# Optimization experiments

Measured on AMD Instinct MI355X. Metric: run time of the kernel, lower is better.

The kernel has to match this reference:

```python
import jax, jax.numpy as jnp
import numpy as np

EMBED_DIM = 1024
NUM_HEADS = 16
WINDOW = 128  # one-sided window length w; total span 2w+1


def setup_inputs() -> dict:
    key = jax.random.key(0)
    ks = jax.random.split(key, 9)
    D = EMBED_DIM
    x = jax.random.normal(ks[0], (2, 8192, D), dtype=jnp.float32)
    s = 0.02
    Wq = jax.random.normal(ks[1], (D, D), dtype=jnp.float32) * s
    bq = jax.random.normal(ks[2], (D,), dtype=jnp.float32) * s
    Wk = jax.random.normal(ks[3], (D, D), dtype=jnp.float32) * s
    bk = jax.random.normal(ks[4], (D,), dtype=jnp.float32) * s
    Wv = jax.random.normal(ks[5], (D, D), dtype=jnp.float32) * s
    bv = jax.random.normal(ks[6], (D,), dtype=jnp.float32) * s
    Wo = jax.random.normal(ks[7], (D, D), dtype=jnp.float32) * s
    bo = jax.random.normal(ks[8], (D,), dtype=jnp.float32) * s
    return {"x": x, "Wq": Wq, "bq": bq, "Wk": Wk, "bk": bk,
            "Wv": Wv, "bv": bv, "Wo": Wo, "bo": bo}


def _sliding_window_attention(x, Wq, bq, Wk, bk, Wv, bv, Wo, bo):
    B, S, D = x.shape
    H, w = NUM_HEADS, WINDOW
    hd = D // H
    bs = w            # block size = window_length; 3 blocks cover [i-w, i+w]
    nb = S // bs

    def proj(W, b):
        y = x @ W.T + b                              # torch Linear: x @ W.T + b
        return y.reshape(B, S, H, hd).transpose(0, 2, 1, 3)  # [B,H,S,hd]

    q = proj(Wq, bq)
    k = proj(Wk, bk)
    v = proj(Wv, bv)

    qb = q.reshape(B, H, nb, bs, hd)
    # pad K/V with one zero block on each side, then build 3-block contexts
    pad = ((0, 0), (0, 0), (bs, bs), (0, 0))
    kp = jnp.pad(k, pad).reshape(B, H, nb + 2, bs, hd)
    vp = jnp.pad(v, pad).reshape(B, H, nb + 2, bs, hd)
    k_ctx = jnp.concatenate([kp[:, :, :-2], kp[:, :, 1:-1], kp[:, :, 2:]], axis=3)  # [B,H,nb,3bs,hd]
    v_ctx = jnp.concatenate([vp[:, :, :-2], vp[:, :, 1:-1], vp[:, :, 2:]], axis=3)

    scale = 1.0 / np.sqrt(hd).astype(np.float32)
    scores = jnp.einsum('bhnqd,bhnkd->bhnqk', qb, k_ctx) * scale  # [B,H,nb,bs,3bs]

    # band mask: |k_pos - q_pos| <= w, and k_pos in [0, S)
    q_off = jnp.arange(bs)
    k_off = jnp.arange(3 * bs)
    rel = k_off[None, :] - bs - q_off[:, None]                # [bs,3bs]
    win_ok = jnp.abs(rel) <= w
    k_pos = (jnp.arange(nb)[:, None, None] - 1) * bs + k_off[None, None, :]
    valid = (k_pos >= 0) & (k_pos < S)                        # [nb,1,3bs]
    mask = win_ok[None] & valid                               # [nb,bs,3bs]

    scores = jnp.where(mask[None, None], scores, jnp.float32(-jnp.inf))
    weights = jax.nn.softmax(scores, axis=-1)

    out = jnp.einsum('bhnqk,bhnkd->bhnqd', weights, v_ctx)    # [B,H,nb,bs,hd]
    out = out.reshape(B, H, S, hd).transpose(0, 2, 1, 3).reshape(B, S, D)
    return out @ Wo.T + bo


def reference(x, Wq, bq, Wk, bk, Wv, bv, Wo, bo):
    return _sliding_window_attention(x, Wq, bq, Wk, bk, Wv, bv, Wo, bo)
```

## Files before the change

kernel.cpp:

```cpp
#include <hip/hip_runtime.h>

typedef __attribute__((ext_vector_type(4))) float f32x4;
typedef __attribute__((ext_vector_type(8))) short s16x8;

#define MFMA16(a, b, c) __builtin_amdgcn_mfma_f32_16x16x32_bf16((a), (b), (c), 0, 0, 0)

__device__ __forceinline__ unsigned short f2bf_bits(float f) {
  unsigned int u = __float_as_uint(f);
  unsigned int r = (u + 0x7fffu + ((u >> 16) & 1u)) >> 16;
  return (unsigned short)r;
}

__device__ __forceinline__ void gl_lds16(const void* g, void* l) {
  __builtin_amdgcn_global_load_lds((const __attribute__((address_space(1))) void*)g,
                                   (__attribute__((address_space(3))) void*)l, 16, 0, 0);
}

__global__ __launch_bounds__(256) void f2bf_kernel(const float* __restrict__ in,
                                                   unsigned short* __restrict__ out, int n4) {
  int idx = blockIdx.x * 256 + threadIdx.x;
  int stride = gridDim.x * 256;
  for (int i = idx; i < n4; i += stride) {
    float4 v = ((const float4*)in)[i];
    ushort4 o;
    o.x = f2bf_bits(v.x); o.y = f2bf_bits(v.y);
    o.z = f2bf_bits(v.z); o.w = f2bf_bits(v.w);
    ((ushort4*)out)[i] = o;
  }
}

__global__ __launch_bounds__(256) void f2bf_w4(const float* __restrict__ w0,
                                               const float* __restrict__ w1,
                                               const float* __restrict__ w2,
                                               const float* __restrict__ w3,
                                               unsigned short* __restrict__ o0,
                                               unsigned short* __restrict__ o1,
                                               unsigned short* __restrict__ o2,
                                               unsigned short* __restrict__ o3) {
  const int s = blockIdx.y;
  const float* in = (s == 0) ? w0 : (s == 1) ? w1 : (s == 2) ? w2 : w3;
  unsigned short* out = (s == 0) ? o0 : (s == 1) ? o1 : (s == 2) ? o2 : o3;
  int i = blockIdx.x * 256 + threadIdx.x;
  float4 v = ((const float4*)in)[i];
  ushort4 o;
  o.x = f2bf_bits(v.x); o.y = f2bf_bits(v.y);
  o.z = f2bf_bits(v.z); o.w = f2bf_bits(v.w);
  ((ushort4*)out)[i] = o;
}


#define S_BARRIER asm volatile("s_barrier" ::: "memory")
#define WAIT_LGKM0 asm volatile("s_waitcnt lgkmcnt(0)" ::: "memory")
#define SCHED_FENCE __builtin_amdgcn_sched_barrier(0)

#define STAGE_HALF(gsrc, ldst)                                                   \
  {                                                                              \
    _Pragma("unroll") for (int i_ = 0; i_ < 2; ++i_) {                           \
      const int ci_ = tid + 512 * i_;                                            \
      const int r_ = ci_ >> 3;                                                   \
      const int c_ = (ci_ & 7) ^ (r_ & 7);                                       \
      gl_lds16((gsrc) + (size_t)r_ * 1024 + c_ * 8, (ldst) + ci_ * 8);           \
    }                                                                            \
  }

#define LDA8(dst, mf_, ks_)                                                      \
  dst = *(const s16x8*)&Ahalf[(((mf_) * 16 + l15) * 8 +                          \
                               (((ks_) * 4 + quad) ^ (l15 & 7))) * 8]
#define LDB8(dst, nf_, ks_)                                                      \
  dst = *(const s16x8*)&Bhalf[((bro + (nf_) * 16 + l15) * 8 +                    \
                               (((ks_) * 4 + quad) ^ (l15 & 7))) * 8]

#define MF_BLOCK(MBASE, NBASE)                                                   \
  _Pragma("unroll") for (int m_ = 0; m_ < 4; ++m_)                               \
    _Pragma("unroll") for (int n_ = 0; n_ < 2; ++n_) {                           \
      acc[(MBASE) + m_][(NBASE) + n_] =                                          \
          MFMA16(af[m_][0], bf[(NBASE) + n_][0], acc[(MBASE) + m_][(NBASE) + n_]); \
      acc[(MBASE) + m_][(NBASE) + n_] =                                          \
          MFMA16(af[m_][1], bf[(NBASE) + n_][1], acc[(MBASE) + m_][(NBASE) + n_]); \
    }

#define GEMM256_CORE(Ab_, Bb_)                                                   \
  f32x4 acc[8][4];                                                               \
  _Pragma("unroll") for (int mi = 0; mi < 8; ++mi)                               \
      _Pragma("unroll") for (int ni = 0; ni < 4; ++ni)                           \
          acc[mi][ni] = (f32x4){0.f, 0.f, 0.f, 0.f};                             \
  {                                                                              \
    s16x8 af[4][2], bf[4][2];                                                    \
                 \
    STAGE_HALF((Ab_), &Al[0][0][0]);                                             \
    STAGE_HALF((Ab_) + 128 * 1024, &Al[0][1][0]);                                \
    STAGE_HALF((Bb_), &Bl[0][0][0]);                                             \
    STAGE_HALF((Bb_) + 128 * 1024, &Bl[0][1][0]);                                \
    STAGE_HALF((Bb_) + 64, &Bl[1][0][0]);                                        \
    STAGE_HALF((Bb_) + 128 * 1024 + 64, &Bl[1][1][0]);                           \
    asm volatile("s_waitcnt vmcnt(4)" ::: "memory");         \
    S_BARRIER;                                                                   \
    _Pragma("unroll 2") for (int T = 0; T < 16; ++T) {                           \
      const int buf_ = T & 1, obuf_ = buf_ ^ 1;                                  \
      const unsigned short* Ahalf = &Al[buf_][wm][0];                            \
      const unsigned short* Bhalf = &Bl[buf_][wn >> 1][0];                       \
          \
      _Pragma("unroll") for (int m_ = 0; m_ < 4; ++m_) {                         \
        LDA8(af[m_][0], m_, 0); LDA8(af[m_][1], m_, 1);                          \
      }                                                                          \
      _Pragma("unroll") for (int n_ = 0; n_ < 2; ++n_) {                         \
        LDB8(bf[n_][0], n_, 0); LDB8(bf[n_][1], n_, 1);                          \
      }                                                                          \
      if (T < 15) STAGE_HALF((Ab_) + (size_t)(T + 1) * 64, &Al[obuf_][0][0]);    \
      S_BARRIER; WAIT_LGKM0; SCHED_FENCE;                                        \
      __builtin_amdgcn_s_setprio(1);                                             \
      MF_BLOCK(0, 0)                                                             \
      __builtin_amdgcn_s_setprio(0);                                             \
      S_BARRIER;                                                                 \
                   \
      _Pragma("unroll") for (int n_ = 2; n_ < 4; ++n_) {                         \
        LDB8(bf[n_][0], n_, 0); LDB8(bf[n_][1], n_, 1);                          \
      }                                                                          \
      if (T < 15)                                                                \
        STAGE_HALF((Ab_) + 128 * 1024 + (size_t)(T + 1) * 64, &Al[obuf_][1][0]); \
      S_BARRIER; WAIT_LGKM0; SCHED_FENCE;                                        \
      __builtin_amdgcn_s_setprio(1);                                             \
      MF_BLOCK(0, 2)                                                             \
      __builtin_amdgcn_s_setprio(0);                                             \
      S_BARRIER;                                                                 \
                   \
      _Pragma("unroll") for (int m_ = 0; m_ < 4; ++m_) {                         \
        LDA8(af[m_][0], 4 + m_, 0); LDA8(af[m_][1], 4 + m_, 1);                  \
      }                                                                          \
      if (T < 14) STAGE_HALF((Bb_) + (size_t)(T + 2) * 64, &Bl[buf_][0][0]);     \
      S_BARRIER; WAIT_LGKM0; SCHED_FENCE;                                        \
      __builtin_amdgcn_s_setprio(1);                                             \
      MF_BLOCK(4, 0)                                                             \
      __builtin_amdgcn_s_setprio(0);                                             \
      S_BARRIER;                                                                 \
                  \
      if (T < 14)                                                                \
        STAGE_HALF((Bb_) + 128 * 1024 + (size_t)(T + 2) * 64, &Bl[buf_][1][0]);  \
      if (T < 14) {                                                              \
        asm volatile("s_waitcnt vmcnt(4)" ::: "memory");                         \
      } else {                                                                   \
        asm volatile("s_waitcnt vmcnt(0)" ::: "memory");                         \
      }                                                                          \
      S_BARRIER; SCHED_FENCE;                                                    \
      __builtin_amdgcn_s_setprio(1);                                             \
      MF_BLOCK(4, 2)                                                             \
      __builtin_amdgcn_s_setprio(0);                                             \
      S_BARRIER;                                                                 \
    }                                                                            \
  }

__global__ __launch_bounds__(512, 2) void gemm_qkv(const unsigned short* __restrict__ A,
                                                   const unsigned short* __restrict__ Wq,
                                                   const unsigned short* __restrict__ Wk,
                                                   const unsigned short* __restrict__ Wv,
                                                   const float* __restrict__ bq,
                                                   const float* __restrict__ bk,
                                                   const float* __restrict__ bv,
                                                   unsigned short* __restrict__ Qo,
                                                   unsigned short* __restrict__ Ko,
                                                   unsigned short* __restrict__ Vt) {
  __shared__ unsigned short Al[2][2][8192];
  __shared__ unsigned short Bl[2][2][8192];
  const int tid = threadIdx.x;
  const int lane = tid & 63, wave = tid >> 6;
  const int l15 = lane & 15, quad = lane >> 4;
  const int wm = wave >> 2, wn = wave & 3;
  const int bro = (wn & 1) * 64;
  const int bx = blockIdx.x;
  const int sel = blockIdx.y >> 2, byl = blockIdx.y & 3;

  const unsigned short* W = (sel == 0) ? Wq : (sel == 1) ? Wk : Wv;
  const float* bias = (sel == 0) ? bq : (sel == 1) ? bk : bv;
  const unsigned short* Ab = A + (size_t)bx * 256 * 1024;
  const unsigned short* Bb = W + (size_t)byl * 256 * 1024;

  GEMM256_CORE(Ab, Bb)

#pragma unroll
  for (int nf = 0; nf < 4; ++nf) {
    const int cn = byl * 256 + wn * 64 + nf * 16 + l15;
    const float bj = bias[cn];
#pragma unroll
    for (int mf = 0; mf < 8; ++mf) {
      const int r0 = bx * 256 + wm * 128 + mf * 16 + quad * 4;
#pragma unroll
      for (int r = 0; r < 4; ++r) {
        const int row = r0 + r;
        const float v = acc[mf][nf][r] + bj;
        if (sel == 0) {
          Qo[(size_t)row * 1024 + cn] = f2bf_bits(v);
        } else if (sel == 1) {
          Ko[(size_t)row * 1024 + cn] = f2bf_bits(v);
        } else {
          Vt[((size_t)(row >> 13) * 1024 + cn) * 8192 + (row & 8191)] = f2bf_bits(v);
        }
      }
    }
  }
}

__global__ __launch_bounds__(512, 2) void gemm_out(const unsigned short* __restrict__ A,
                                                   const unsigned short* __restrict__ B,
                                                   const float* __restrict__ bias,
                                                   float* __restrict__ Cf) {
  __shared__ unsigned short Al[2][2][8192];
  __shared__ unsigned short Bl[2][2][8192];
  const int tid = threadIdx.x;
  const int lane = tid & 63, wave = tid >> 6;
  const int l15 = lane & 15, quad = lane >> 4;
  const int wm = wave >> 2, wn = wave & 3;
  const int bro = (wn & 1) * 64;
  const int bx = blockIdx.x;

  const unsigned short* Ab = A + (size_t)bx * 256 * 1024;
  const unsigned short* Bb = B + (size_t)blockIdx.y * 256 * 1024;

  GEMM256_CORE(Ab, Bb)

#pragma unroll
  for (int nf = 0; nf < 4; ++nf) {
    const int cn = blockIdx.y * 256 + wn * 64 + nf * 16 + l15;
    const float bj = bias[cn];
#pragma unroll
    for (int mf = 0; mf < 8; ++mf) {
      const int r0 = bx * 256 + wm * 128 + mf * 16 + quad * 4;
#pragma unroll
      for (int r = 0; r < 4; ++r) Cf[(size_t)(r0 + r) * 1024 + cn] = acc[mf][nf][r] + bj;
    }
  }
}

__global__ __launch_bounds__(256, 3) void attn_kernel(const unsigned short* __restrict__ Q,
                                                      const unsigned short* __restrict__ Km,
                                                      const unsigned short* __restrict__ Vt,
                                                      unsigned short* __restrict__ O) {
  const int n = blockIdx.x;
  const int bh = blockIdx.y;
  const int b = bh >> 4, h = bh & 15;
  const int tid = threadIdx.x, lane = tid & 63, wave = tid >> 6;
  const int l15 = lane & 15, quad = lane >> 4;

  __shared__ unsigned short Kl[384 * 64];
  __shared__ unsigned short Ps[4][16 * 40];

  const int base_row = n * 128 - 128;

  for (int i = 0; i < 12; ++i) {
    const int c = i * 256 + tid;
    const int row = c >> 3;
    const int qc = (c & 7) ^ (row & 7);
    int gr = base_row + row;
    gr = min(max(gr, 0), 8191);
    gl_lds16(Km + (size_t)(b * 8192 + gr) * 1024 + h * 64 + qc * 8, &Kl[c * 8]);
  }
  __syncthreads();

  const unsigned short* Vbase = Vt + (size_t)bh * 64 * 8192;
  unsigned short* strip = &Ps[wave][0];

  for (int mt = 0; mt < 2; ++mt) {
    const int qt = wave * 2 + mt;
    const int q0 = n * 128 + qt * 16;
    const int qp = q0 + l15;

    const unsigned short* qptr = Q + (size_t)(b * 8192 + qp) * 1024 + h * 64 + quad * 8;
    const s16x8 bq0 = *(const s16x8*)qptr;
    const s16x8 bq1 = *(const s16x8*)(qptr + 32);

    f32x4 o[4];
#pragma unroll
    for (int dt = 0; dt < 4; ++dt) o[dt] = (f32x4){0.f, 0.f, 0.f, 0.f};
    float lsum = 0.f;

    const int krel0 = qt * 16;

#pragma unroll 1
    for (int p = 0; p < 9; ++p) {
      f32x4 st[2];
#pragma unroll
      for (int tt = 0; tt < 2; ++tt) {
        int rel = krel0 + p * 32 + tt * 16 + l15;
        int rr = min(rel, 383);
        const int ro = rr * 8;
        const int sw = rr & 7;
        const s16x8 ka0 = *(const s16x8*)&Kl[(ro + (quad ^ sw)) * 8];
        const s16x8 ka1 = *(const s16x8*)&Kl[(ro + ((4 + quad) ^ sw)) * 8];
        f32x4 a = (f32x4){0.f, 0.f, 0.f, 0.f};
        a = MFMA16(ka0, bq0, a);
        a = MFMA16(ka1, bq1, a);
        st[tt] = a;
      }
      ushort4 w0, w1;
#pragma unroll
      for (int tt = 0; tt < 2; ++tt) {
        unsigned short* wp = tt ? (unsigned short*)&w1 : (unsigned short*)&w0;
#pragma unroll
        for (int r = 0; r < 4; ++r) {
          const int kp = base_row + krel0 + p * 32 + tt * 16 + quad * 4 + r;
          const int dd = kp - qp;
          const bool ok = (kp >= 0) && (kp < 8192) && (dd >= -128) && (dd <= 128);
          const float pv = ok ? __expf(st[tt][r] * 0.125f) : 0.f;
          lsum += pv;
          wp[r] = f2bf_bits(pv);
        }
      }
      *(ushort4*)&strip[l15 * 40 + quad * 4] = w0;
      *(ushort4*)&strip[l15 * 40 + 16 + quad * 4] = w1;
      const s16x8 pf = *(const s16x8*)&strip[l15 * 40 + quad * 8];
      int kc = base_row + krel0 + p * 32 + quad * 8;
      kc = min(max(kc, 0), 8184);
#pragma unroll
      for (int dt = 0; dt < 4; ++dt) {
        const s16x8 va = *(const s16x8*)(Vbase + (size_t)(dt * 16 + l15) * 8192 + kc);
        o[dt] = MFMA16(va, pf, o[dt]);
      }
    }

    lsum += __shfl_xor(lsum, 16, 64);
    lsum += __shfl_xor(lsum, 32, 64);
    const float rinv = 1.f / lsum;
    unsigned short* obase = O + (size_t)(b * 8192 + qp) * 1024 + h * 64;
#pragma unroll
    for (int dt = 0; dt < 4; ++dt) {
      ushort4 w;
      unsigned short* wp = (unsigned short*)&w;
#pragma unroll
      for (int r = 0; r < 4; ++r) wp[r] = f2bf_bits(o[dt][r] * rinv);
      *(ushort4*)(obase + dt * 16 + quad * 4) = w;
    }
  }
}

extern "C" void kernel_launch(void* const* d_in, const int* in_sizes, int n_in, void* d_out,
                              int out_size, void* d_ws, size_t ws_size, hipStream_t stream) {
  const float* x = (const float*)d_in[0];
  const float* Wq = (const float*)d_in[1];
  const float* bq = (const float*)d_in[2];
  const float* Wk = (const float*)d_in[3];
  const float* bk = (const float*)d_in[4];
  const float* Wv = (const float*)d_in[5];
  const float* bv = (const float*)d_in[6];
  const float* Wo = (const float*)d_in[7];
  const float* bo = (const float*)d_in[8];
  float* out = (float*)d_out;

  const int M = 16384, D = 1024;

  unsigned short* xb = (unsigned short*)d_ws;
  unsigned short* qb = xb + (size_t)M * D;
  unsigned short* kb = qb + (size_t)M * D;
  unsigned short* vt = kb + (size_t)M * D;
  unsigned short* ab = vt + (size_t)M * D;
  unsigned short* wqb = ab + (size_t)M * D;
  unsigned short* wkb = wqb + (size_t)D * D;
  unsigned short* wvb = wkb + (size_t)D * D;
  unsigned short* wob = wvb + (size_t)D * D;

  f2bf_kernel<<<16384, 256, 0, stream>>>(x, xb, M * D / 4);
  f2bf_w4<<<dim3(1024, 4), 256, 0, stream>>>(Wq, Wk, Wv, Wo, wqb, wkb, wvb, wob);

  gemm_qkv<<<dim3(M / 256, 12), 512, 0, stream>>>(xb, wqb, wkb, wvb, bq, bk, bv, qb, kb, vt);

  attn_kernel<<<dim3(64, 32), 256, 0, stream>>>(qb, kb, vt, ab);

  gemm_out<<<dim3(M / 256, D / 256), 512, 0, stream>>>(ab, wob, bo, out);
}
```

Measured before the change: 418.8 us.

## Software-pipeline GEMM LDS fragment reads across phases with precomputed ds_read offsets

```diff
diff --git a/kernel.cpp b/kernel.cpp
--- a/kernel.cpp
+++ b/kernel.cpp
@@ -14,6 +14,17 @@
 __device__ __forceinline__ void gl_lds16(const void* g, void* l) {
   __builtin_amdgcn_global_load_lds((const __attribute__((address_space(1))) void*)g,
                                    (__attribute__((address_space(3))) void*)l, 16, 0, 0);
+}
+
+__device__ __forceinline__ unsigned lds_off(const void* p) {
+  return (unsigned)(unsigned long long)p;
+}
+
+template <int IMM>
+__device__ __forceinline__ s16x8 dsr(unsigned base) {
+  s16x8 r;
+  asm volatile("ds_read_b128 %0, %1 offset:%2" : "=v"(r) : "v"(base), "n"(IMM));
+  return r;
 }
 
 __global__ __launch_bounds__(256) void f2bf_kernel(const float* __restrict__ in,
@@ -49,104 +60,142 @@
 }
 
 
-#define S_BARRIER asm volatile("s_barrier" ::: "memory")
-#define WAIT_LGKM0 asm volatile("s_waitcnt lgkmcnt(0)" ::: "memory")
+#define S_BAR __builtin_amdgcn_s_barrier()
+#define WAIT_LGKM0 asm volatile("s_waitcnt lgkmcnt(0)")
 #define SCHED_FENCE __builtin_amdgcn_sched_barrier(0)
-
-#define STAGE_HALF(gsrc, ldst)                                                   \
-  {                                                                              \
-    _Pragma("unroll") for (int i_ = 0; i_ < 2; ++i_) {                           \
-      const int ci_ = tid + 512 * i_;                                            \
-      const int r_ = ci_ >> 3;                                                   \
-      const int c_ = (ci_ & 7) ^ (r_ & 7);                                       \
-      gl_lds16((gsrc) + (size_t)r_ * 1024 + c_ * 8, (ldst) + ci_ * 8);           \
-    }                                                                            \
-  }
-
-#define LDA8(dst, mf_, ks_)                                                      \
-  dst = *(const s16x8*)&Ahalf[(((mf_) * 16 + l15) * 8 +                          \
-                               (((ks_) * 4 + quad) ^ (l15 & 7))) * 8]
-#define LDB8(dst, nf_, ks_)                                                      \
-  dst = *(const s16x8*)&Bhalf[((bro + (nf_) * 16 + l15) * 8 +                    \
-                               (((ks_) * 4 + quad) ^ (l15 & 7))) * 8]
-
-#define MF_BLOCK(MBASE, NBASE)                                                   \
-  _Pragma("unroll") for (int m_ = 0; m_ < 4; ++m_)                               \
-    _Pragma("unroll") for (int n_ = 0; n_ < 2; ++n_) {                           \
-      acc[(MBASE) + m_][(NBASE) + n_] =                                          \
-          MFMA16(af[m_][0], bf[(NBASE) + n_][0], acc[(MBASE) + m_][(NBASE) + n_]); \
-      acc[(MBASE) + m_][(NBASE) + n_] =                                          \
-          MFMA16(af[m_][1], bf[(NBASE) + n_][1], acc[(MBASE) + m_][(NBASE) + n_]); \
+#define PRIO1 __builtin_amdgcn_s_setprio(1)
+#define PRIO0 __builtin_amdgcn_s_setprio(0)
+
+#define STAGE2(gsrc, ldsdst)                                    \
+  gl_lds16((gsrc), (ldsdst) + (size_t)tid * 8);                 \
+  gl_lds16((gsrc) + 65536, (ldsdst) + (size_t)tid * 8 + 4096);
+
+#define RD_A03(ax0, ax1)                                        \
+  afA[0][0] = dsr<0>(ax0);      afA[0][1] = dsr<0>(ax1);        \
+  afA[1][0] = dsr<2048>(ax0);   afA[1][1] = dsr<2048>(ax1);     \
+  afA[2][0] = dsr<4096>(ax0);   afA[2][1] = dsr<4096>(ax1);     \
+  afA[3][0] = dsr<6144>(ax0);   afA[3][1] = dsr<6144>(ax1);
+#define RD_A47(ax0, ax1)                                        \
+  afB[0][0] = dsr<8192>(ax0);   afB[0][1] = dsr<8192>(ax1);     \
+  afB[1][0] = dsr<10240>(ax0);  afB[1][1] = dsr<10240>(ax1);    \
+  afB[2][0] = dsr<12288>(ax0);  afB[2][1] = dsr<12288>(ax1);    \
+  afB[3][0] = dsr<14336>(ax0);  afB[3][1] = dsr<14336>(ax1);
+#define RD_B01(bx0, bx1)                                        \
+  bf[0][0] = dsr<0>(bx0);       bf[0][1] = dsr<0>(bx1);         \
+  bf[1][0] = dsr<2048>(bx0);    bf[1][1] = dsr<2048>(bx1);
+#define RD_B23(bx0, bx1)                                        \
+  bf[2][0] = dsr<4096>(bx0);    bf[2][1] = dsr<4096>(bx1);      \
+  bf[3][0] = dsr<6144>(bx0);    bf[3][1] = dsr<6144>(bx1);
+
+#define MM_BLOCK(AF, MB, NB)                                                          \
+  _Pragma("unroll") for (int m_ = 0; m_ < 4; ++m_)                                    \
+    _Pragma("unroll") for (int n_ = 0; n_ < 2; ++n_) {                                \
+      acc[(MB) + m_][(NB) + n_] =                                                     \
+          MFMA16(AF[m_][0], bf[(NB) + n_][0], acc[(MB) + m_][(NB) + n_]);             \
+      acc[(MB) + m_][(NB) + n_] =                                                     \
+          MFMA16(AF[m_][1], bf[(NB) + n_][1], acc[(MB) + m_][(NB) + n_]);             \
     }
 
-#define GEMM256_CORE(Ab_, Bb_)                                                   \
-  f32x4 acc[8][4];                                                               \
-  _Pragma("unroll") for (int mi = 0; mi < 8; ++mi)                               \
-      _Pragma("unroll") for (int ni = 0; ni < 4; ++ni)                           \
-          acc[mi][ni] = (f32x4){0.f, 0.f, 0.f, 0.f};                             \
-  {                                                                              \
-    s16x8 af[4][2], bf[4][2];                                                    \
-                 \
-    STAGE_HALF((Ab_), &Al[0][0][0]);                                             \
-    STAGE_HALF((Ab_) + 128 * 1024, &Al[0][1][0]);                                \
-    STAGE_HALF((Bb_), &Bl[0][0][0]);                                             \
-    STAGE_HALF((Bb_) + 128 * 1024, &Bl[0][1][0]);                                \
-    STAGE_HALF((Bb_) + 64, &Bl[1][0][0]);                                        \
-    STAGE_HALF((Bb_) + 128 * 1024 + 64, &Bl[1][1][0]);                           \
-    asm volatile("s_waitcnt vmcnt(4)" ::: "memory");         \
-    S_BARRIER;                                                                   \
-    _Pragma("unroll 2") for (int T = 0; T < 16; ++T) {                           \
-      const int buf_ = T & 1, obuf_ = buf_ ^ 1;                                  \
-      const unsigned short* Ahalf = &Al[buf_][wm][0];                            \
-      const unsigned short* Bhalf = &Bl[buf_][wn >> 1][0];                       \
-          \
-      _Pragma("unroll") for (int m_ = 0; m_ < 4; ++m_) {                         \
-        LDA8(af[m_][0], m_, 0); LDA8(af[m_][1], m_, 1);                          \
-      }                                                                          \
-      _Pragma("unroll") for (int n_ = 0; n_ < 2; ++n_) {                         \
-        LDB8(bf[n_][0], n_, 0); LDB8(bf[n_][1], n_, 1);                          \
-      }                                                                          \
-      if (T < 15) STAGE_HALF((Ab_) + (size_t)(T + 1) * 64, &Al[obuf_][0][0]);    \
-      S_BARRIER; WAIT_LGKM0; SCHED_FENCE;                                        \
-      __builtin_amdgcn_s_setprio(1);                                             \
-      MF_BLOCK(0, 0)                                                             \
-      __builtin_amdgcn_s_setprio(0);                                             \
-      S_BARRIER;                                                                 \
+#define TILE_FULL(T_, AC0, AC1, AO0, AO1, BC0, BC1, BO0, BO1, ALO_, BLC_)  \
+  S_BAR; WAIT_LGKM0; SCHED_FENCE; PRIO1;                                   \
+  RD_B23(BC0, BC1);                                                        \
+  STAGE2(gA + ((T_) + 1) * 64, (ALO_));                                    \
+  MM_BLOCK(afA, 0, 0);                                                     \
+  PRIO0;                                                                   \
+  S_BAR; WAIT_LGKM0; SCHED_FENCE; PRIO1;                                   \
+  RD_A47(AC0, AC1);                                                        \
+  STAGE2(gA + 131072 + ((T_) + 1) * 64, (ALO_) + 8192);                    \
+  MM_BLOCK(afA, 0, 2);                                                     \
+  PRIO0;                                                                   \
+  S_BAR; WAIT_LGKM0; SCHED_FENCE; PRIO1;                                   \
+  STAGE2(gB + ((T_) + 2) * 64, (BLC_));                                    \
+  MM_BLOCK(afB, 4, 0);                                                     \
+  PRIO0; SCHED_FENCE;                                                      \
+  asm volatile("s_waitcnt vmcnt(2)");                                      \
+  S_BAR; SCHED_FENCE; PRIO1;                                               \
+  RD_A03(AO0, AO1);                                                        \
+  RD_B01(BO0, BO1);                                                        \
+  STAGE2(gB + 131072 + ((T_) + 2) * 64, (BLC_) + 8192);                    \
+  MM_BLOCK(afB, 4, 2);                                                     \
+  PRIO0;
+
+#define GEMM256_CORE(Ab_, Bb_)                                                        \
+  f32x4 acc[8][4];                                                                    \
+  _Pragma("unroll") for (int mi = 0; mi < 8; ++mi)                                    \
+      _Pragma("unroll") for (int ni = 0; ni < 4; ++ni)                                \
+          acc[mi][ni] = (f32x4){0.f, 0.f, 0.f, 0.f};                                  \
+  s16x8 afA[4][2], afB[4][2], bf[4][2];                                               \
+  {                                                                                   \
+    const int r_ = tid >> 3;                                                          \
+    const int c_ = (tid & 7) ^ (r_ & 7);                                              \
+    const unsigned short* gA = (Ab_) + (size_t)r_ * 1024 + c_ * 8;                    \
+    const unsigned short* gB = (Bb_) + (size_t)r_ * 1024 + c_ * 8;                    \
+    const unsigned x0 = (unsigned)((quad ^ (l15 & 7)) * 16);                          \
+    const unsigned x1 = (unsigned)(((4 + quad) ^ (l15 & 7)) * 16);                    \
+    const unsigned aW = (unsigned)(l15 * 128);                                        \
+    const unsigned bW = (unsigned)(bro * 128 + l15 * 128);                            \
+    const unsigned a0x0 = lds_off(&Al[0][wm][0]) + aW + x0;                           \
+    const unsigned a0x1 = lds_off(&Al[0][wm][0]) + aW + x1;                           \
+    const unsigned a1x0 = lds_off(&Al[1][wm][0]) + aW + x0;                           \
+    const unsigned a1x1 = lds_off(&Al[1][wm][0]) + aW + x1;                           \
+    const unsigned b0x0 = lds_off(&Bl[0][wn >> 1][0]) + bW + x0;                      \
+    const unsigned b0x1 = lds_off(&Bl[0][wn >> 1][0]) + bW + x1;                      \
+    const unsigned b1x0 = lds_off(&Bl[1][wn >> 1][0]) + bW + x0;                      \
+    const unsigned b1x1 = lds_off(&Bl[1][wn >> 1][0]) + bW + x1;                      \
                    \
-      _Pragma("unroll") for (int n_ = 2; n_ < 4; ++n_) {                         \
-        LDB8(bf[n_][0], n_, 0); LDB8(bf[n_][1], n_, 1);                          \
-      }                                                                          \
-      if (T < 15)                                                                \
-        STAGE_HALF((Ab_) + 128 * 1024 + (size_t)(T + 1) * 64, &Al[obuf_][1][0]); \
-      S_BARRIER; WAIT_LGKM0; SCHED_FENCE;                                        \
-      __builtin_amdgcn_s_setprio(1);                                             \
-      MF_BLOCK(0, 2)                                                             \
-      __builtin_amdgcn_s_setprio(0);                                             \
-      S_BARRIER;                                                                 \
+    STAGE2(gA, (&Al[0][0][0]));                                                       \
+    STAGE2(gA + 131072, (&Al[0][0][0]) + 8192);                                       \
+    STAGE2(gB, (&Bl[0][0][0]));                                                       \
+    STAGE2(gB + 131072, (&Bl[0][0][0]) + 8192);                                       \
+    STAGE2(gB + 64, (&Bl[1][0][0]));                                                  \
+    STAGE2(gB + 131072 + 64, (&Bl[1][0][0]) + 8192);                                  \
+    SCHED_FENCE;                                                                      \
+    asm volatile("s_waitcnt vmcnt(4)");           \
+    S_BAR; SCHED_FENCE;                                                               \
+    RD_A03(a0x0, a0x1);                                                               \
+    RD_B01(b0x0, b0x1);                                                               \
+    _Pragma("unroll 1") for (int Tp = 0; Tp < 7; ++Tp) {                              \
+      const int T0 = Tp * 2;                                                          \
+      TILE_FULL(T0, a0x0, a0x1, a1x0, a1x1, b0x0, b0x1, b1x0, b1x1,                   \
+                (&Al[1][0][0]), (&Bl[0][0][0]));                                      \
+      TILE_FULL(T0 + 1, a1x0, a1x1, a0x0, a0x1, b1x0, b1x1, b0x0, b0x1,               \
+                (&Al[0][0][0]), (&Bl[1][0][0]));                                      \
+    }                                                                                 \
                    \
-      _Pragma("unroll") for (int m_ = 0; m_ < 4; ++m_) {                         \
-        LDA8(af[m_][0], 4 + m_, 0); LDA8(af[m_][1], 4 + m_, 1);                  \
-      }                                                                          \
-      if (T < 14) STAGE_HALF((Bb_) + (size_t)(T + 2) * 64, &Bl[buf_][0][0]);     \
-      S_BARRIER; WAIT_LGKM0; SCHED_FENCE;                                        \
-      __builtin_amdgcn_s_setprio(1);                                             \
-      MF_BLOCK(4, 0)                                                             \
-      __builtin_amdgcn_s_setprio(0);                                             \
-      S_BARRIER;                                                                 \
-                  \
-      if (T < 14)                                                                \
-        STAGE_HALF((Bb_) + 128 * 1024 + (size_t)(T + 2) * 64, &Bl[buf_][1][0]);  \
-      if (T < 14) {                                                              \
-        asm volatile("s_waitcnt vmcnt(4)" ::: "memory");                         \
-      } else {                                                                   \
-        asm volatile("s_waitcnt vmcnt(0)" ::: "memory");                         \
-      }                                                                          \
-      S_BARRIER; SCHED_FENCE;                                                    \
-      __builtin_amdgcn_s_setprio(1);                                             \
-      MF_BLOCK(4, 2)                                                             \
-      __builtin_amdgcn_s_setprio(0);                                             \
-      S_BARRIER;                                                                 \
-    }                                                                            \
+    S_BAR; WAIT_LGKM0; SCHED_FENCE; PRIO1;                                            \
+    RD_B23(b0x0, b0x1);                                                               \
+    STAGE2(gA + 15 * 64, (&Al[1][0][0]));                                             \
+    MM_BLOCK(afA, 0, 0);                                                              \
+    PRIO0;                                                                            \
+    S_BAR; WAIT_LGKM0; SCHED_FENCE; PRIO1;                                            \
+    RD_A47(a0x0, a0x1);                                                               \
+    STAGE2(gA + 131072 + 15 * 64, (&Al[1][0][0]) + 8192);                             \
+    MM_BLOCK(afA, 0, 2);                                                              \
+    PRIO0;                                                                            \
+    S_BAR; WAIT_LGKM0; SCHED_FENCE; PRIO1;                                            \
+    MM_BLOCK(afB, 4, 0);                                                              \
+    PRIO0; SCHED_FENCE;                                                               \
+    asm volatile("s_waitcnt vmcnt(0)");                                               \
+    S_BAR; SCHED_FENCE; PRIO1;                                                        \
+    RD_A03(a1x0, a1x1);                                                               \
+    RD_B01(b1x0, b1x1);                                                               \
+    MM_BLOCK(afB, 4, 2);                                                              \
+    PRIO0;                                                                            \
+                                    \
+    S_BAR; WAIT_LGKM0; SCHED_FENCE; PRIO1;                                            \
+    RD_B23(b1x0, b1x1);                                                               \
+    MM_BLOCK(afA, 0, 0);                                                              \
+    PRIO0;                                                                            \
+    S_BAR; WAIT_LGKM0; SCHED_FENCE; PRIO1;                                            \
+    RD_A47(a1x0, a1x1);                                                               \
+    MM_BLOCK(afA, 0, 2);                                                              \
+    PRIO0;                                                                            \
+    S_BAR; WAIT_LGKM0; SCHED_FENCE; PRIO1;                                            \
+    MM_BLOCK(afB, 4, 0);                                                              \
+    PRIO0;                                                                            \
+    S_BAR; SCHED_FENCE; PRIO1;                                                        \
+    MM_BLOCK(afB, 4, 2);                                                              \
+    PRIO0;                                                                            \
   }
 
 __global__ __launch_bounds__(512, 2) void gemm_qkv(const unsigned short* __restrict__ A,
```

Result: faster. 408.0 us (-2.6%).
